# Kernel tuning notes

Hardware: AMD Instinct MI355X
Metric: run time of the kernel (lower is better)

## Reference

```python
import jax, jax.numpy as jnp
import numpy as np

EPS = 1e-5

def _layernorm(x, g, b):
    mu = jnp.mean(x, axis=-1, keepdims=True)
    var = jnp.mean((x - mu) ** 2, axis=-1, keepdims=True)
    return (x - mu) * jax.lax.rsqrt(var + EPS) * g + b

def setup_inputs() -> dict:
    key = jax.random.key(0)
    ks = jax.random.split(key, 12)
    B, N, C, n = 2, 1024, 256, 100
    x = jax.random.normal(ks[0], (B, N, C), dtype=jnp.float32)
    query = jax.random.normal(ks[1], (n, B, C), dtype=jnp.float32)
    policy = jax.random.uniform(ks[2], (B, N, 1), dtype=jnp.float32)
    s = lambda k, shp: jax.random.normal(k, shp, dtype=jnp.float32) * (1.0 / np.sqrt(shp[0]))
    return {
        "x": x, "query": query, "policy": policy,
        "ln_g": jnp.ones((C,), jnp.float32), "ln_b": jnp.zeros((C,), jnp.float32),
        "W_in": s(ks[3], (C, C)), "b_in": jnp.zeros((C,), jnp.float32),
        "W1": s(ks[4], (2 * C, C)), "b1": jnp.zeros((C,), jnp.float32),
        "W2": s(ks[5], (C, C // 2)), "b2": jnp.zeros((C // 2,), jnp.float32),
        "W3": s(ks[6], (C // 2, 2)), "b3": jnp.zeros((2,), jnp.float32),
    }

def reference(x, query, policy, ln_g, ln_b, W_in, b_in, W1, b1, W2, b2, W3, b3):
    B, N, C = x.shape
    n = query.shape[0]
    q = jnp.transpose(query, (1, 0, 2))  # [B, n, C]
    # in_conv: LayerNorm -> Linear -> GELU. The torch code repeats x across the
    # query dim first, but the math is identical per query, so compute once.
    h = jax.nn.gelu(_layernorm(x, ln_g, ln_b) @ W_in + b_in, approximate=False)  # [B, N, C]
    half = C // 2
    local_x = h[:, :, :half]  # [B, N, C/2]
    # policy-weighted masked pooling (policy identical across queries)
    glob = jnp.sum(h[:, :, half:] * policy, axis=1, keepdims=True) / jnp.sum(policy, axis=1, keepdims=True)  # [B, 1, C/2]
    feature = jnp.concatenate([
        jnp.broadcast_to(local_x[:, None, :, :], (B, n, N, half)),
        jnp.broadcast_to(glob[:, None, :, :], (B, n, N, half)),
        jnp.broadcast_to(q[:, :, None, :], (B, n, N, C)),
    ], axis=-1)  # [B, n, N, 2C]
    z = jax.nn.gelu(feature @ W1 + b1, approximate=False)
    z = jax.nn.gelu(z @ W2 + b2, approximate=False)
    z = z @ W3 + b3
    return jax.nn.log_softmax(z, axis=-1)  # [B, n, N, 2]
```

## Files before the change

### kernel.cpp

```cpp
#include <hip/hip_runtime.h>
#include <math.h>

#define BB 2
#define NN 1024
#define CC 256
#define NQ 100
#define HALF 128

typedef __attribute__((ext_vector_type(8))) short bf16x8;
typedef __attribute__((ext_vector_type(4))) float f32x4;

__device__ __forceinline__ float gelu_fast(float x) {
    float a = fabsf(0.70710678118654752f * x);
    float t = fmaf(a, 4.30638e-5f, 2.765672e-4f);
    t = fmaf(a, t, 1.520143e-4f);
    t = fmaf(a, t, 9.2705272e-3f);
    t = fmaf(a, t, 4.22820123e-2f);
    t = fmaf(a, t, 7.05230784e-2f);
    float p = fmaf(a, t, 1.0f);
    float p2 = p * p;
    float p4 = p2 * p2;
    float p8 = p4 * p4;
    float p16 = p8 * p8;
    float r = 0.5f * __builtin_amdgcn_rcpf(p16);
    float phi = (x >= 0.0f) ? (1.0f - r) : r;
    return x * phi;
}

__device__ __forceinline__ short f2bf(float f) {
    union { float f; unsigned u; } v; v.f = f;
    return (short)((v.u + 0x7FFFu + ((v.u >> 16) & 1u)) >> 16);
}

__global__ __launch_bounds__(256) void kA_fused(
        const float* __restrict__ x, const float* __restrict__ ln_g,
        const float* __restrict__ ln_b, const float* __restrict__ W_in,
        const float* __restrict__ b_in, const float* __restrict__ policy,
        const float* __restrict__ W1, const float* __restrict__ W2,
        float* __restrict__ At, float* __restrict__ gpart,
        float* __restrict__ ppart, short* __restrict__ W2T) {
    int t = threadIdx.x;
    int blk = blockIdx.x;
    if (blk >= 512) {
        int u = (blk - 512) * 256 + t;
        int c = u >> 6, kg = u & 63;
        short4 v;
        v.x = f2bf(W2[(kg * 4 + 0) * HALF + c]);
        v.y = f2bf(W2[(kg * 4 + 1) * HALF + c]);
        v.z = f2bf(W2[(kg * 4 + 2) * HALF + c]);
        v.w = f2bf(W2[(kg * 4 + 3) * HALF + c]);
        *(short4*)(W2T + c * CC + kg * 4) = v;
        return;
    }
    __shared__ float xst[CC][4];
    __shared__ float hst[HALF][4];
    int wave = t >> 6, lane = t & 63;
    int row0 = blk * 4;
    const float* xr = x + (size_t)(row0 + wave) * CC;
    float v0 = xr[lane], v1 = xr[lane + 64], v2 = xr[lane + 128], v3 = xr[lane + 192];
    float s = v0 + v1 + v2 + v3;
    for (int off = 32; off; off >>= 1) s += __shfl_down(s, off);
    s = __shfl(s, 0);
    float mu = s * (1.0f / CC);
    float d0 = v0 - mu, d1 = v1 - mu, d2 = v2 - mu, d3 = v3 - mu;
    float vs = d0 * d0 + d1 * d1 + d2 * d2 + d3 * d3;
    for (int off = 32; off; off >>= 1) vs += __shfl_down(vs, off);
    vs = __shfl(vs, 0);
    float rstd = rsqrtf(vs * (1.0f / CC) + 1e-5f);
    xst[lane][wave]       = d0 * rstd * ln_g[lane]       + ln_b[lane];
    xst[lane + 64][wave]  = d1 * rstd * ln_g[lane + 64]  + ln_b[lane + 64];
    xst[lane + 128][wave] = d2 * rstd * ln_g[lane + 128] + ln_b[lane + 128];
    xst[lane + 192][wave] = d3 * rstd * ln_g[lane + 192] + ln_b[lane + 192];
    __syncthreads();
    float a0 = b_in[t], a1 = a0, a2 = a0, a3 = a0;
    #pragma unroll 8
    for (int k = 0; k < CC; ++k) {
        float4 xv = *(const float4*)xst[k];
        float wv = W_in[k * CC + t];
        a0 = fmaf(xv.x, wv, a0); a1 = fmaf(xv.y, wv, a1);
        a2 = fmaf(xv.z, wv, a2); a3 = fmaf(xv.w, wv, a3);
    }
    float h0 = gelu_fast(a0), h1 = gelu_fast(a1), h2 = gelu_fast(a2), h3 = gelu_fast(a3);
    float p0 = policy[row0], p1 = policy[row0 + 1], p2 = policy[row0 + 2], p3 = policy[row0 + 3];
    if (t < HALF) {
        hst[t][0] = h0; hst[t][1] = h1; hst[t][2] = h2; hst[t][3] = h3;
    } else {
        gpart[(size_t)blk * HALF + (t - HALF)] = h0 * p0 + h1 * p1 + h2 * p2 + h3 * p3;
    }
    if (t == 0) ppart[blk] = p0 + p1 + p2 + p3;
    __syncthreads();
    float c0 = 0, c1 = 0, c2 = 0, c3 = 0;
    #pragma unroll 8
    for (int k = 0; k < HALF; ++k) {
        float4 hv = *(const float4*)hst[k];
        float wv = W1[k * CC + t];
        c0 = fmaf(hv.x, wv, c0); c1 = fmaf(hv.y, wv, c1);
        c2 = fmaf(hv.z, wv, c2); c3 = fmaf(hv.w, wv, c3);
    }
    int b = row0 >> 10;
    int lr = row0 & (NN - 1);
    size_t tb = ((size_t)(b * 64 + (lr >> 4)) * 32 + (t >> 3)) * 128 + (t & 7);
    int r16 = lr & 15;
    At[tb + (r16 + 0) * 8] = c0;
    At[tb + (r16 + 1) * 8] = c1;
    At[tb + (r16 + 2) * 8] = c2;
    At[tb + (r16 + 3) * 8] = c3;
}

__global__ __launch_bounds__(256) void kB_qc(
        const float* __restrict__ query, const float* __restrict__ W1,
        const float* __restrict__ gpart, const float* __restrict__ ppart,
        const float* __restrict__ b1, float* __restrict__ Qc) {
    __shared__ float gls[HALF];
    __shared__ float qs[CC];
    __shared__ float psS;
    int blk = blockIdx.x, t = threadIdx.x;
    int b = blk / NQ, i = blk % NQ;
    if (t < 64) {
        const float* pp = ppart + b * 256;
        float ps = pp[t] + pp[t + 64] + pp[t + 128] + pp[t + 192];
        for (int off = 32; off; off >>= 1) ps += __shfl_down(ps, off);
        if (t == 0) psS = ps;
    }
    if (t < HALF) {
        const float* gp = gpart + (size_t)b * 256 * HALF + t;
        float s = 0.f;
        #pragma unroll 8
        for (int ch = 0; ch < 256; ++ch) s += gp[ch * HALF];
        gls[t] = s;
    }
    qs[t] = query[(size_t)(i * BB + b) * CC + t];
    __syncthreads();
    float inv_ps = 1.0f / psS;
    float g = b1[t];
    #pragma unroll 8
    for (int k = 0; k < HALF; ++k)
        g = fmaf(gls[k] * inv_ps, W1[(HALF + k) * CC + t], g);
    #pragma unroll 8
    for (int k = 0; k < CC; ++k)
        g = fmaf(qs[k], W1[(2 * HALF + k) * CC + t], g);
    Qc[(size_t)blk * CC + t] = g;
}

#define W2S 40

__global__ __launch_bounds__(256, 6) void k5_main(
        const float* __restrict__ At, const float* __restrict__ Qc,
        const short* __restrict__ W2T, const float* __restrict__ b2,
        const float* __restrict__ W3, const float* __restrict__ b3,
        float* __restrict__ out) {
    __shared__ short w2s[2][128 * W2S];

    int t = threadIdx.x;
    int lane = t & 63, w = t >> 6;
    int col16 = lane & 15, quad = lane >> 4;
    int blk = blockIdx.x;
    int jt = blk & 15;
    int iq = (blk >> 4) % NQ;
    int b  = blk / (16 * NQ);
    const float* Abase = At + ((size_t)(b * 64 + jt * 4 + w) * 32) * 128 + col16 * 8;
    const float* Qrow = Qc + (size_t)(b * NQ + iq) * CC;

    int sn = t >> 2, skg = t & 3;
    const short* Wg0 = W2T + sn * CC + skg * 8;
    const short* Wg1 = W2T + (64 + sn) * CC + skg * 8;
    short* Ws0 = (short*)w2s + sn * W2S + skg * 8;
    short* Ws1 = (short*)w2s + (64 + sn) * W2S + skg * 8;

    f32x4 acc[8];
    #pragma unroll
    for (int ni = 0; ni < 8; ++ni) acc[ni] = (f32x4){0.f, 0.f, 0.f, 0.f};

    {
        bf16x8 r0 = *(const bf16x8*)(Wg0);
        bf16x8 r1 = *(const bf16x8*)(Wg1);
        *(bf16x8*)(Ws0) = r0;
        *(bf16x8*)(Ws1) = r1;
    }
    __syncthreads();

    #pragma unroll
    for (int kt = 0; kt < 8; ++kt) {
        int buf = kt & 1;
        bf16x8 nx0, nx1;
        if (kt < 7) {
            nx0 = *(const bf16x8*)(Wg0 + (kt + 1) * 32);
            nx1 = *(const bf16x8*)(Wg1 + (kt + 1) * 32);
        }
        int k0 = kt * 32 + quad * 8;
        float4 q0 = *(const float4*)(Qrow + k0);
        float4 q1 = *(const float4*)(Qrow + k0 + 4);
        const float* Ap = Abase + (size_t)(kt * 4 + quad) * 128;
        float4 a0 = *(const float4*)(Ap);
        float4 a1 = *(const float4*)(Ap + 4);
        union { bf16x8 v; short s[8]; } u;
        u.s[0] = f2bf(gelu_fast(a0.x + q0.x));
        u.s[1] = f2bf(gelu_fast(a0.y + q0.y));
        u.s[2] = f2bf(gelu_fast(a0.z + q0.z));
        u.s[3] = f2bf(gelu_fast(a0.w + q0.w));
        u.s[4] = f2bf(gelu_fast(a1.x + q1.x));
        u.s[5] = f2bf(gelu_fast(a1.y + q1.y));
        u.s[6] = f2bf(gelu_fast(a1.z + q1.z));
        u.s[7] = f2bf(gelu_fast(a1.w + q1.w));
        #pragma unroll
        for (int ni = 0; ni < 8; ++ni) {
            bf16x8 bfv = *(const bf16x8*)&w2s[buf][(ni * 16 + col16) * W2S + quad * 8];
            acc[ni] = __builtin_amdgcn_mfma_f32_16x16x32_bf16(u.v, bfv, acc[ni], 0, 0, 0);
        }
        if (kt < 7) {
            short* d0 = Ws0 + (1 - buf) * 128 * W2S;
            short* d1 = Ws1 + (1 - buf) * 128 * W2S;
            *(bf16x8*)d0 = nx0;
            *(bf16x8*)d1 = nx1;
            __syncthreads();
        }
    }

    float p0[4] = {0, 0, 0, 0}, p1[4] = {0, 0, 0, 0};
    #pragma unroll
    for (int ni = 0; ni < 8; ++ni) {
        int c = ni * 16 + col16;
        float bb = b2[c];
        float2 w3v = *(const float2*)(W3 + c * 2);
        #pragma unroll
        for (int r = 0; r < 4; ++r) {
            float z = gelu_fast(acc[ni][r] + bb);
            p0[r] = fmaf(z, w3v.x, p0[r]);
            p1[r] = fmaf(z, w3v.y, p1[r]);
        }
    }
    float b30 = b3[0], b31 = b3[1];
    #pragma unroll
    for (int r = 0; r < 4; ++r) {
        float s0 = p0[r], s1 = p1[r];
        #pragma unroll
        for (int off = 1; off < 16; off <<= 1) {
            s0 += __shfl_xor(s0, off);
            s1 += __shfl_xor(s1, off);
        }
        if (col16 == 0) {
            float z0 = s0 + b30, z1v = s1 + b31;
            float m = fmaxf(z0, z1v);
            float lse = m + __logf(__expf(z0 - m) + __expf(z1v - m));
            int j = jt * 64 + w * 16 + quad * 4 + r;
            *(float2*)(out + ((size_t)(b * NQ + iq) * NN + j) * 2) =
                make_float2(z0 - lse, z1v - lse);
        }
    }
}

extern "C" void kernel_launch(void* const* d_in, const int* in_sizes, int n_in,
                              void* d_out, int out_size, void* d_ws, size_t ws_size,
                              hipStream_t stream) {
    const float* x      = (const float*)d_in[0];
    const float* query  = (const float*)d_in[1];
    const float* policy = (const float*)d_in[2];
    const float* ln_g   = (const float*)d_in[3];
    const float* ln_b   = (const float*)d_in[4];
    const float* W_in   = (const float*)d_in[5];
    const float* b_in   = (const float*)d_in[6];
    const float* W1     = (const float*)d_in[7];
    const float* b1     = (const float*)d_in[8];
    const float* W2     = (const float*)d_in[9];
    const float* b2     = (const float*)d_in[10];
    const float* W3     = (const float*)d_in[11];
    const float* b3     = (const float*)d_in[12];
    float* out = (float*)d_out;

    float* ws    = (float*)d_ws;
    float* At    = ws;
    float* Qc    = ws + 524288;
    float* gpart = ws + 575488;
    float* ppart = ws + 641024;
    short* W2T   = (short*)(ws + 641536);

    kA_fused<<<544, 256, 0, stream>>>(x, ln_g, ln_b, W_in, b_in, policy,
                                      W1, W2, At, gpart, ppart, W2T);
    kB_qc<<<BB * NQ, 256, 0, stream>>>(query, W1, gpart, ppart, b1, Qc);
    k5_main<<<BB * NQ * (NN / 64), 256, 0, stream>>>(At, Qc, W2T, b2, W3, b3, out);
}
```

Measured before the change: 174.6 us.

## Pre-swizzle W2T into MFMA fragment order and read B directly from global

```diff
diff --git a/kernel.cpp b/kernel.cpp
--- a/kernel.cpp
+++ b/kernel.cpp
@@ -43,13 +43,14 @@
     int blk = blockIdx.x;
     if (blk >= 512) {
         int u = (blk - 512) * 256 + t;
-        int c = u >> 6, kg = u & 63;
+        int n = u >> 6, kg = u & 63;
         short4 v;
-        v.x = f2bf(W2[(kg * 4 + 0) * HALF + c]);
-        v.y = f2bf(W2[(kg * 4 + 1) * HALF + c]);
-        v.z = f2bf(W2[(kg * 4 + 2) * HALF + c]);
-        v.w = f2bf(W2[(kg * 4 + 3) * HALF + c]);
-        *(short4*)(W2T + c * CC + kg * 4) = v;
+        v.x = f2bf(W2[(kg * 4 + 0) * HALF + n]);
+        v.y = f2bf(W2[(kg * 4 + 1) * HALF + n]);
+        v.z = f2bf(W2[(kg * 4 + 2) * HALF + n]);
+        v.w = f2bf(W2[(kg * 4 + 3) * HALF + n]);
+        *(short4*)(W2T + ((size_t)((n >> 4) * 32 + (kg >> 1)) * 128
+                          + (n & 15) * 8 + (kg & 1) * 4)) = v;
         return;
     }
     __shared__ float xst[CC][4];
@@ -142,15 +143,11 @@
     Qc[(size_t)blk * CC + t] = g;
 }
 
-#define W2S 40
-
 __global__ __launch_bounds__(256, 6) void k5_main(
         const float* __restrict__ At, const float* __restrict__ Qc,
         const short* __restrict__ W2T, const float* __restrict__ b2,
         const float* __restrict__ W3, const float* __restrict__ b3,
         float* __restrict__ out) {
-    __shared__ short w2s[2][128 * W2S];
-
     int t = threadIdx.x;
     int lane = t & 63, w = t >> 6;
     int col16 = lane & 15, quad = lane >> 4;
@@ -160,33 +157,14 @@
     int b  = blk / (16 * NQ);
     const float* Abase = At + ((size_t)(b * 64 + jt * 4 + w) * 32) * 128 + col16 * 8;
     const float* Qrow = Qc + (size_t)(b * NQ + iq) * CC;
-
-    int sn = t >> 2, skg = t & 3;
-    const short* Wg0 = W2T + sn * CC + skg * 8;
-    const short* Wg1 = W2T + (64 + sn) * CC + skg * 8;
-    short* Ws0 = (short*)w2s + sn * W2S + skg * 8;
-    short* Ws1 = (short*)w2s + (64 + sn) * W2S + skg * 8;
+    const short* Bbase = W2T + (size_t)quad * 128 + col16 * 8;
 
     f32x4 acc[8];
     #pragma unroll
     for (int ni = 0; ni < 8; ++ni) acc[ni] = (f32x4){0.f, 0.f, 0.f, 0.f};
 
-    {
-        bf16x8 r0 = *(const bf16x8*)(Wg0);
-        bf16x8 r1 = *(const bf16x8*)(Wg1);
-        *(bf16x8*)(Ws0) = r0;
-        *(bf16x8*)(Ws1) = r1;
-    }
-    __syncthreads();
-
     #pragma unroll
     for (int kt = 0; kt < 8; ++kt) {
-        int buf = kt & 1;
-        bf16x8 nx0, nx1;
-        if (kt < 7) {
-            nx0 = *(const bf16x8*)(Wg0 + (kt + 1) * 32);
-            nx1 = *(const bf16x8*)(Wg1 + (kt + 1) * 32);
-        }
         int k0 = kt * 32 + quad * 8;
         float4 q0 = *(const float4*)(Qrow + k0);
         float4 q1 = *(const float4*)(Qrow + k0 + 4);
@@ -202,17 +180,11 @@
         u.s[5] = f2bf(gelu_fast(a1.y + q1.y));
         u.s[6] = f2bf(gelu_fast(a1.z + q1.z));
         u.s[7] = f2bf(gelu_fast(a1.w + q1.w));
+        const short* Bk = Bbase + (size_t)(kt * 4) * 128;
         #pragma unroll
         for (int ni = 0; ni < 8; ++ni) {
-            bf16x8 bfv = *(const bf16x8*)&w2s[buf][(ni * 16 + col16) * W2S + quad * 8];
+            bf16x8 bfv = *(const bf16x8*)(Bk + (size_t)ni * 32 * 128);
             acc[ni] = __builtin_amdgcn_mfma_f32_16x16x32_bf16(u.v, bfv, acc[ni], 0, 0, 0);
-        }
-        if (kt < 7) {
-            short* d0 = Ws0 + (1 - buf) * 128 * W2S;
-            short* d1 = Ws1 + (1 - buf) * 128 * W2S;
-            *(bf16x8*)d0 = nx0;
-            *(bf16x8*)d1 = nx1;
-            __syncthreads();
         }
     }
 
```

Result: slower. 185.2 us (+6.1%).
